# Kernel optimization log

Measured on AMD Instinct MI355X. Metric: run time of the kernel, lower is better.

## Reference

```python
import jax, jax.numpy as jnp
import numpy as np
from jax import lax

EPS = 1e-5

def setup_inputs() -> dict:
    key = jax.random.key(0)
    k1, k2, k3, k4, k5, k6 = jax.random.split(key, 6)
    x = jax.random.normal(k1, (1, 64, 31, 96, 96), dtype=jnp.float32)
    # small init scale keeps gate pre-activations in a sane range
    w = jax.random.normal(k2, (256, 64, 3, 3, 3), dtype=jnp.float32) * 0.05
    gamma = jax.random.uniform(k3, (256,), dtype=jnp.float32)
    beta = jax.random.normal(k4, (256,), dtype=jnp.float32) * 0.1
    mean = jax.random.normal(k5, (256,), dtype=jnp.float32) * 0.1
    var = jax.random.uniform(k6, (256,), dtype=jnp.float32) + 0.5
    return {"x": x, "w": w, "gamma": gamma, "beta": beta, "mean": mean, "var": var}

def _bcast(p):
    return p[None, :, None, None, None]

def reference(x, w, gamma, beta, mean, var):
    # Conv3d (bias=False), stride 1, padding 1, NCDHW
    gates = lax.conv_general_dilated(
        x, w, window_strides=(1, 1, 1), padding=[(1, 1)] * 3,
        dimension_numbers=("NCDHW", "OIDHW", "NCDHW"))
    # BatchNorm3d (inference, running stats)
    scale = gamma * lax.rsqrt(var + EPS)
    gates = gates * _bcast(scale) + _bcast(beta - mean * scale)
    C = 64  # out_channels
    Wx = jnp.tanh(gates[:, 0 * C:1 * C])
    ft = jax.nn.sigmoid(gates[:, 1 * C:2 * C])
    rt = jax.nn.sigmoid(gates[:, 2 * C:3 * C])
    X = jnp.tanh(gates[:, 3 * C:4 * C])  # act == 'tanh'
    # time axis (dim 2) to front: (D, B, C, H, W)
    Wt = jnp.moveaxis(Wx, 2, 0)
    Ft = jnp.moveaxis(ft, 2, 0)
    Rt = jnp.moveaxis(rt, 2, 0)
    Xt = jnp.moveaxis(X, 2, 0)
    # t = 0: Ct = 1 - ft (note: Wx unused at first step, per source)
    C0 = 1.0 - Ft[0]
    h0 = Rt[0] * C0 + (1.0 - Rt[0]) * Xt[0]
    def step(Ct, inp):
        wx, f, r, xx = inp
        Ct = f * Ct + (1.0 - f) * wx
        ht = r * Ct + (1.0 - r) * xx
        return Ct, ht
    _, hs = lax.scan(step, C0, (Wt[1:], Ft[1:], Rt[1:], Xt[1:]))
    hts = jnp.concatenate([h0[None], hs], axis=0)  # (D,B,C,H,W)
    return jnp.moveaxis(hts, 0, 2)  # (B,C,D,H,W)
```

## Files before the change

kernel.cpp:

```cpp
#include <hip/hip_runtime.h>
#include <cstddef>

#define CI_  64
#define CO_  256
#define DD_  31
#define HH_  96
#define WW_  96
#define HW_  (HH_*WW_)
#define DHW_ (DD_*HW_)
#define EPSV 1e-5f

#define PD_   33
#define PH_   98
#define PW_   98
#define PHW_  9604
#define PDHW_ 316932

#define S_COL 8
#define S_CIG 144
#define S_ROW 1152
#define S_DD  11520
#define NTASK 4320
#define NTASKP 4352
#define XH_N  (NTASKP*8)

#define NTILE 72
#define NBLK  (NTILE*DD_)
#define GSP   128

typedef _Float16 half8   __attribute__((ext_vector_type(8)));
typedef _Float16 half4v  __attribute__((ext_vector_type(4)));
typedef float    float4v __attribute__((ext_vector_type(4)));

__device__ __forceinline__ void gl_lds16(const _Float16* g, _Float16* l) {
  __builtin_amdgcn_global_load_lds(
      (const __attribute__((address_space(1))) unsigned int*)(g),
      (__attribute__((address_space(3))) unsigned int*)(l), 16, 0, 0);
}

__global__ __launch_bounds__(256) void repack_w_k(const float* __restrict__ w,
                                                  _Float16* __restrict__ wr2) {
  int idx = blockIdx.x * 256 + threadIdx.x;
  if (idx >= 55296) return;
  int lw   = idx & 15;
  int quad = (idx >> 4) & 3;
  int cog  = (idx >> 6) & 15;
  int tkc  = idx >> 10;
  int kc   = tkc & 1;
  int t    = tkc >> 1;
  int co   = cog * 16 + lw;
  int cib  = kc * 32 + quad * 8;
  half8 v;
#pragma unroll
  for (int s = 0; s < 8; s++)
    v[s] = (_Float16)w[(size_t)co * 1728 + (size_t)(cib + s) * 27 + t];
  *(half8*)(wr2 + (size_t)idx * 8) = v;
}

__global__ __launch_bounds__(256) void pad_zero_k(_Float16* __restrict__ xt) {
  int p = blockIdx.x * 256 + threadIdx.x;
  if (p >= PDHW_) return;
  int pd  = p / PHW_;
  int rem = p - pd * PHW_;
  int ph  = rem / PW_;
  int pw  = rem - ph * PW_;
  bool in = (pd >= 1) & (pd <= DD_) & (ph >= 1) & (ph <= HH_) & (pw >= 1) & (pw <= WW_);
  if (in) return;
  half8 z = (half8)(_Float16)0.f;
#pragma unroll
  for (int cig = 0; cig < 8; cig++)
    *(half8*)(xt + ((size_t)cig * PDHW_ + p) * 8) = z;
}

__global__ __launch_bounds__(256) void transpose_x_k(const float* __restrict__ x,
                                                     _Float16* __restrict__ xt) {
  int idx = blockIdx.x * 256 + threadIdx.x;
  if (idx >= 31 * 96 * 24) return;
  int wq  = idx % 24;
  int rem = idx / 24;
  int h   = rem % 96;
  int d   = rem / 96;
  const float* xp = x + (size_t)d * HW_ + (size_t)h * WW_ + wq * 4;
  size_t p0 = (size_t)(d + 1) * PHW_ + (size_t)(h + 1) * PW_ + (wq * 4 + 1);
#pragma unroll 1
  for (int cig = 0; cig < 8; cig++) {
    float4 vv[8];
#pragma unroll
    for (int s = 0; s < 8; s++)
      vv[s] = *(const float4*)(xp + (size_t)(cig * 8 + s) * DHW_);
#pragma unroll
    for (int k = 0; k < 4; k++) {
      half8 o;
#pragma unroll
      for (int s = 0; s < 8; s++) o[s] = (_Float16)(&vv[s].x)[k];
      *(half8*)(xt + ((size_t)cig * PDHW_ + p0 + k) * 8) = o;
    }
  }
}

__global__ __launch_bounds__(512, 4) void conv_mfma_k(
    const _Float16* __restrict__ xt, const _Float16* __restrict__ wr2,
    const float* __restrict__ gamma, const float* __restrict__ beta,
    const float* __restrict__ mean, const float* __restrict__ var,
    _Float16* __restrict__ gates)
{
  __shared__ _Float16 xh[XH_N];

  const int bid  = blockIdx.x;
  const int flat = (bid & 7) * 279 + (bid >> 3);
  const int d    = flat / NTILE;
  const int bx   = flat - d * NTILE;
  const int wti  = bx % 6;
  const int hti  = bx / 6;
  const int h0   = hti * 8, w0 = wti * 16;

  const int tid  = threadIdx.x;
  const int lane = tid & 63;
  const int wave = __builtin_amdgcn_readfirstlane(tid >> 6);
  const int wm   = wave >> 2;
  const int wn   = wave & 3;
  const int lw   = lane & 15;
  const int quad = lane >> 4;

#pragma unroll 1
  for (int it = 0; it < 9; ++it) {
    const int wb = it * 512 + wave * 64;
    if (wb < NTASKP) {
      const int task = wb + lane;
      const int tt   = task < NTASK ? task : (NTASK - 1);
      int col = tt % 18;
      int rc  = tt / 18;
      int cig = rc & 7;
      int dr  = rc >> 3;
      int dd  = dr / 10;
      int row = dr - dd * 10;
      const _Float16* g = xt + (((size_t)cig * PDHW_ + (size_t)(d + dd) * PHW_ +
                                 (size_t)(h0 + row) * PW_ + (w0 + col)) << 3);
      gl_lds16(g, xh + (size_t)wb * 8);
    }
  }

  float4v acc[4][4];
#pragma unroll
  for (int m = 0; m < 4; m++)
#pragma unroll
    for (int j = 0; j < 4; j++) acc[m][j] = (float4v)0.f;

  __syncthreads();

  const int abase0 = quad * S_CIG + lw * S_COL + (wm * 4) * S_ROW;

#define LOADB(bf, s)                                                          \
  {                                                                           \
    const int t9_ = (s) / 6, sub_ = (s) - 6 * t9_;                            \
    const int kc_ = sub_ / 3, kw_ = sub_ - 3 * kc_;                           \
    const int t_  = t9_ * 3 + kw_;                                            \
    const _Float16* bp_ =                                                     \
        wr2 + (((size_t)((t_ * 2 + kc_) * 16 + wn * 4)) << 9) + (lane << 3);  \
    bf[0] = *(const half8*)(bp_);                                             \
    bf[1] = *(const half8*)(bp_ + (1 << 9));                                  \
    bf[2] = *(const half8*)(bp_ + (2 << 9));                                  \
    bf[3] = *(const half8*)(bp_ + (3 << 9));                                  \
  }

#define STEP(s, bf)                                                           \
  {                                                                           \
    const int t9_ = (s) / 6, sub_ = (s) - 6 * t9_;                            \
    const int kc_ = sub_ / 3, kw_ = sub_ - 3 * kc_;                           \
    const int kd_ = t9_ / 3, kh_ = t9_ - 3 * kd_;                             \
    const int ab_ = abase0 + kd_ * S_DD + kh_ * S_ROW + kc_ * (4 * S_CIG) +   \
                    kw_ * S_COL;                                              \
    half8 af0 = *(const half8*)(xh + ab_);                                    \
    half8 af1 = *(const half8*)(xh + ab_ + S_ROW);                            \
    half8 af2 = *(const half8*)(xh + ab_ + 2 * S_ROW);                        \
    half8 af3 = *(const half8*)(xh + ab_ + 3 * S_ROW);                        \
    __builtin_amdgcn_s_setprio(1);                                            \
    _Pragma("unroll")                                                         \
    for (int j = 0; j < 4; ++j) {                                             \
      acc[0][j] = __builtin_amdgcn_mfma_f32_16x16x32_f16(af0, bf[j], acc[0][j], 0, 0, 0); \
      acc[1][j] = __builtin_amdgcn_mfma_f32_16x16x32_f16(af1, bf[j], acc[1][j], 0, 0, 0); \
      acc[2][j] = __builtin_amdgcn_mfma_f32_16x16x32_f16(af2, bf[j], acc[2][j], 0, 0, 0); \
      acc[3][j] = __builtin_amdgcn_mfma_f32_16x16x32_f16(af3, bf[j], acc[3][j], 0, 0, 0); \
    }                                                                         \
    __builtin_amdgcn_s_setprio(0);                                            \
  }

  half8 bfa[4], bfb[4];
  LOADB(bfa, 0)
#pragma unroll 1
  for (int i = 0; i < 27; ++i) {
    const int s0 = 2 * i;
    LOADB(bfb, s0 + 1)
    STEP(s0, bfa)
    if (i < 26) LOADB(bfa, s0 + 2)
    STEP(s0 + 1, bfb)
  }
#undef LOADB
#undef STEP

  _Float16* gb = gates + ((size_t)(d * NTILE + bx) * 256) * GSP;
#pragma unroll
  for (int j = 0; j < 4; j++) {
    const int co = wn * 64 + j * 16 + lw;
    const float s  = gamma[co] * rsqrtf(var[co] + EPSV);
    const float bb = fmaf(-mean[co], s, beta[co]);
#pragma unroll
    for (int m = 0; m < 4; m++) {
      half4v hv;
#pragma unroll
      for (int reg = 0; reg < 4; reg++)
        hv[reg] = (_Float16)fmaf(acc[m][j][reg], s, bb);
      *(half4v*)(gb + (size_t)co * GSP + (wm * 4 + m) * 16 + quad * 4) = hv;
    }
  }
}

__device__ __forceinline__ float tanh_f(float v) {
  float t = __expf(-2.f * fabsf(v));
  return copysignf((1.f - t) * __builtin_amdgcn_rcpf(1.f + t), v);
}
__device__ __forceinline__ float sigm_f(float v) {
  return __builtin_amdgcn_rcpf(1.f + __expf(-v));
}

__global__ __launch_bounds__(256) void recurrence_k(const _Float16* __restrict__ gates,
                                                    float* __restrict__ out) {
  const int idx = blockIdx.x * 256 + threadIdx.x;
  const int q   = idx & 31;
  const int t2  = idx >> 5;
  const int c   = t2 / NTILE;
  const int bx  = t2 - c * NTILE;
  const int hti = bx / 6, wti = bx - hti * 6;
  const int sp  = q * 4;
  const int h   = hti * 8 + (sp >> 4);
  const int w   = wti * 16 + (sp & 15);

  const size_t DSTR = (size_t)NTILE * 256 * GSP;
  const _Float16* g0 = gates + (size_t)bx * 256 * GSP + sp;
  float* op = out + (size_t)c * DHW_ + (size_t)h * WW_ + w;

#define LD(dv, gate) (*(const half4v*)(g0 + (size_t)(dv) * DSTR + (size_t)(c + ((gate) << 6)) * GSP))

  half4v cf = LD(0, 1), cr = LD(0, 2), cx = LD(0, 3);
  half4v nwx = LD(1, 0), nf = LD(1, 1), nr = LD(1, 2), nx = LD(1, 3);
  float C[4];
  {
    float4 st;
#pragma unroll
    for (int k = 0; k < 4; k++) {
      C[k] = 1.f - sigm_f((float)cf[k]);
      float r0 = sigm_f((float)cr[k]), x0 = tanh_f((float)cx[k]);
      (&st.x)[k] = fmaf(r0, C[k] - x0, x0);
    }
    *(float4*)op = st;
  }
#pragma unroll 1
  for (int d = 1; d < DD_; d++) {
    half4v cwx = nwx; cf = nf; cr = nr; cx = nx;
    if (d < DD_ - 1) {
      nwx = LD(d + 1, 0); nf = LD(d + 1, 1);
      nr  = LD(d + 1, 2); nx = LD(d + 1, 3);
    }
    float4 st;
#pragma unroll
    for (int k = 0; k < 4; k++) {
      float wx0 = tanh_f((float)cwx[k]);
      float f0  = sigm_f((float)cf[k]);
      float r0  = sigm_f((float)cr[k]);
      float x0  = tanh_f((float)cx[k]);
      C[k] = fmaf(f0, C[k] - wx0, wx0);
      (&st.x)[k] = fmaf(r0, C[k] - x0, x0);
    }
    *(float4*)(op + (size_t)d * HW_) = st;
  }
#undef LD
}

extern "C" void kernel_launch(void* const* d_in, const int* in_sizes, int n_in,
                              void* d_out, int out_size, void* d_ws, size_t ws_size,
                              hipStream_t stream) {
  const float* x     = (const float*)d_in[0];
  const float* w     = (const float*)d_in[1];
  const float* gamma = (const float*)d_in[2];
  const float* beta  = (const float*)d_in[3];
  const float* mean  = (const float*)d_in[4];
  const float* var   = (const float*)d_in[5];
  float* out = (float*)d_out;

  _Float16* wr2   = (_Float16*)d_ws;
  _Float16* xt    = (_Float16*)((char*)d_ws + 884736);
  _Float16* gates = (_Float16*)((char*)d_ws + 884736 + 40567296);

  repack_w_k<<<216, 256, 0, stream>>>(w, wr2);
  pad_zero_k<<<(PDHW_ + 255) / 256, 256, 0, stream>>>(xt);
  transpose_x_k<<<(31 * 96 * 24 + 255) / 256, 256, 0, stream>>>(x, xt);
  conv_mfma_k<<<NBLK, 512, 0, stream>>>(xt, wr2, gamma, beta, mean, var, gates);
  recurrence_k<<<(64 * NTILE * 32) / 256, 256, 0, stream>>>(gates, out);
}
```

Measured before the change: 421.5 us.

## Fuse prep kernels and move gate activations into conv epilogue with LDS-staged stores

Merges the weight repack, pad zeroing and input transpose into one launch that dispatches by block index. It moves the tanh/sigmoid activations from the recurrence kernel into the conv epilogue, where they run once per gate element rather than inside the serial time loop. Gate stores are staged through swizzled LDS so each lane writes contiguous half8 chunks to global memory, replacing scattered half4 writes. The epilogue gains an extra __syncthreads and LDS traffic, and activations are now rounded to fp16 after being computed rather than before.

```diff
diff --git a/kernel.cpp b/kernel.cpp
--- a/kernel.cpp
+++ b/kernel.cpp
@@ -28,6 +28,11 @@
 #define NBLK  (NTILE*DD_)
 #define GSP   128
 
+#define PREP_RB 216
+#define PREP_PB 1239
+#define PREP_TB 279
+#define PREP_NB (PREP_RB + PREP_PB + PREP_TB)
+
 typedef _Float16 half8   __attribute__((ext_vector_type(8)));
 typedef _Float16 half4v  __attribute__((ext_vector_type(4)));
 typedef float    float4v __attribute__((ext_vector_type(4)));
@@ -38,64 +43,71 @@
       (__attribute__((address_space(3))) unsigned int*)(l), 16, 0, 0);
 }
 
-__global__ __launch_bounds__(256) void repack_w_k(const float* __restrict__ w,
-                                                  _Float16* __restrict__ wr2) {
-  int idx = blockIdx.x * 256 + threadIdx.x;
-  if (idx >= 55296) return;
-  int lw   = idx & 15;
-  int quad = (idx >> 4) & 3;
-  int cog  = (idx >> 6) & 15;
-  int tkc  = idx >> 10;
-  int kc   = tkc & 1;
-  int t    = tkc >> 1;
-  int co   = cog * 16 + lw;
-  int cib  = kc * 32 + quad * 8;
-  half8 v;
-#pragma unroll
-  for (int s = 0; s < 8; s++)
-    v[s] = (_Float16)w[(size_t)co * 1728 + (size_t)(cib + s) * 27 + t];
-  *(half8*)(wr2 + (size_t)idx * 8) = v;
-}
-
-__global__ __launch_bounds__(256) void pad_zero_k(_Float16* __restrict__ xt) {
-  int p = blockIdx.x * 256 + threadIdx.x;
-  if (p >= PDHW_) return;
-  int pd  = p / PHW_;
-  int rem = p - pd * PHW_;
-  int ph  = rem / PW_;
-  int pw  = rem - ph * PW_;
-  bool in = (pd >= 1) & (pd <= DD_) & (ph >= 1) & (ph <= HH_) & (pw >= 1) & (pw <= WW_);
-  if (in) return;
-  half8 z = (half8)(_Float16)0.f;
-#pragma unroll
-  for (int cig = 0; cig < 8; cig++)
-    *(half8*)(xt + ((size_t)cig * PDHW_ + p) * 8) = z;
-}
-
-__global__ __launch_bounds__(256) void transpose_x_k(const float* __restrict__ x,
-                                                     _Float16* __restrict__ xt) {
-  int idx = blockIdx.x * 256 + threadIdx.x;
-  if (idx >= 31 * 96 * 24) return;
-  int wq  = idx % 24;
-  int rem = idx / 24;
-  int h   = rem % 96;
-  int d   = rem / 96;
-  const float* xp = x + (size_t)d * HW_ + (size_t)h * WW_ + wq * 4;
-  size_t p0 = (size_t)(d + 1) * PHW_ + (size_t)(h + 1) * PW_ + (wq * 4 + 1);
+__global__ __launch_bounds__(256) void prep_k(const float* __restrict__ w,
+                                              const float* __restrict__ x,
+                                              _Float16* __restrict__ wr2,
+                                              _Float16* __restrict__ xt) {
+  const int bid = blockIdx.x;
+  if (bid < PREP_RB) {
+    int idx = bid * 256 + threadIdx.x;
+    int lw   = idx & 15;
+    int quad = (idx >> 4) & 3;
+    int cog  = (idx >> 6) & 15;
+    int tkc  = idx >> 10;
+    int kc   = tkc & 1;
+    int t    = tkc >> 1;
+    int co   = cog * 16 + lw;
+    int cib  = kc * 32 + quad * 8;
+    half8 v;
+#pragma unroll
+    for (int s = 0; s < 8; s++)
+      v[s] = (_Float16)w[(size_t)co * 1728 + (size_t)(cib + s) * 27 + t];
+    *(half8*)(wr2 + (size_t)idx * 8) = v;
+  } else if (bid < PREP_RB + PREP_PB) {
+    int p = (bid - PREP_RB) * 256 + threadIdx.x;
+    if (p >= PDHW_) return;
+    int pd  = p / PHW_;
+    int rem = p - pd * PHW_;
+    int ph  = rem / PW_;
+    int pw  = rem - ph * PW_;
+    bool in = (pd >= 1) & (pd <= DD_) & (ph >= 1) & (ph <= HH_) & (pw >= 1) & (pw <= WW_);
+    if (in) return;
+    half8 z = (half8)(_Float16)0.f;
+#pragma unroll
+    for (int cig = 0; cig < 8; cig++)
+      *(half8*)(xt + ((size_t)cig * PDHW_ + p) * 8) = z;
+  } else {
+    int idx = (bid - PREP_RB - PREP_PB) * 256 + threadIdx.x;
+    if (idx >= 31 * 96 * 24) return;
+    int wq  = idx % 24;
+    int rem = idx / 24;
+    int h   = rem % 96;
+    int d   = rem / 96;
+    const float* xp = x + (size_t)d * HW_ + (size_t)h * WW_ + wq * 4;
+    size_t p0 = (size_t)(d + 1) * PHW_ + (size_t)(h + 1) * PW_ + (wq * 4 + 1);
 #pragma unroll 1
-  for (int cig = 0; cig < 8; cig++) {
-    float4 vv[8];
-#pragma unroll
-    for (int s = 0; s < 8; s++)
-      vv[s] = *(const float4*)(xp + (size_t)(cig * 8 + s) * DHW_);
-#pragma unroll
-    for (int k = 0; k < 4; k++) {
-      half8 o;
-#pragma unroll
-      for (int s = 0; s < 8; s++) o[s] = (_Float16)(&vv[s].x)[k];
-      *(half8*)(xt + ((size_t)cig * PDHW_ + p0 + k) * 8) = o;
-    }
-  }
+    for (int cig = 0; cig < 8; cig++) {
+      float4 vv[8];
+#pragma unroll
+      for (int s = 0; s < 8; s++)
+        vv[s] = *(const float4*)(xp + (size_t)(cig * 8 + s) * DHW_);
+#pragma unroll
+      for (int k = 0; k < 4; k++) {
+        half8 o;
+#pragma unroll
+        for (int s = 0; s < 8; s++) o[s] = (_Float16)(&vv[s].x)[k];
+        *(half8*)(xt + ((size_t)cig * PDHW_ + p0 + k) * 8) = o;
+      }
+    }
+  }
+}
+
+__device__ __forceinline__ float tanh_f(float v) {
+  float t = __expf(-2.f * fabsf(v));
+  return copysignf((1.f - t) * __builtin_amdgcn_rcpf(1.f + t), v);
+}
+__device__ __forceinline__ float sigm_f(float v) {
+  return __builtin_amdgcn_rcpf(1.f + __expf(-v));
 }
 
 __global__ __launch_bounds__(512, 4) void conv_mfma_k(
@@ -198,29 +210,38 @@
 #undef LOADB
 #undef STEP
 
-  _Float16* gb = gates + ((size_t)(d * NTILE + bx) * 256) * GSP;
+  __syncthreads();
+
+  _Float16* wt = xh + wave * 4096;
+  const bool istanh = (wn == 0) || (wn == 3);
 #pragma unroll
   for (int j = 0; j < 4; j++) {
-    const int co = wn * 64 + j * 16 + lw;
+    const int co  = wn * 64 + j * 16 + lw;
+    const int col = j * 16 + lw;
     const float s  = gamma[co] * rsqrtf(var[co] + EPSV);
     const float bb = fmaf(-mean[co], s, beta[co]);
+    const int key = (col & 7) << 3;
 #pragma unroll
     for (int m = 0; m < 4; m++) {
       half4v hv;
 #pragma unroll
-      for (int reg = 0; reg < 4; reg++)
-        hv[reg] = (_Float16)fmaf(acc[m][j][reg], s, bb);
-      *(half4v*)(gb + (size_t)co * GSP + (wm * 4 + m) * 16 + quad * 4) = hv;
-    }
-  }
-}
-
-__device__ __forceinline__ float tanh_f(float v) {
-  float t = __expf(-2.f * fabsf(v));
-  return copysignf((1.f - t) * __builtin_amdgcn_rcpf(1.f + t), v);
-}
-__device__ __forceinline__ float sigm_f(float v) {
-  return __builtin_amdgcn_rcpf(1.f + __expf(-v));
+      for (int reg = 0; reg < 4; reg++) {
+        float v = fmaf(acc[m][j][reg], s, bb);
+        float a;
+        if (istanh) a = tanh_f(v); else a = sigm_f(v);
+        hv[reg] = (_Float16)a;
+      }
+      *(half4v*)(wt + col * 64 + ((m * 16 + quad * 4) ^ key)) = hv;
+    }
+  }
+  _Float16* gb = gates + ((size_t)(d * NTILE + bx) * 256 + wn * 64) * GSP + wm * 64;
+  const int rb = (lane & 7) * 8;
+#pragma unroll
+  for (int s8 = 0; s8 < 8; s8++) {
+    const int col = s8 * 8 + (lane >> 3);
+    half8 rv = *(const half8*)(wt + col * 64 + (rb ^ ((col & 7) << 3)));
+    *(half8*)(gb + (size_t)col * GSP + rb) = rv;
+  }
 }
 
 __global__ __launch_bounds__(256) void recurrence_k(const _Float16* __restrict__ gates,
@@ -248,8 +269,8 @@
     float4 st;
 #pragma unroll
     for (int k = 0; k < 4; k++) {
-      C[k] = 1.f - sigm_f((float)cf[k]);
-      float r0 = sigm_f((float)cr[k]), x0 = tanh_f((float)cx[k]);
+      C[k] = 1.f - (float)cf[k];
+      float r0 = (float)cr[k], x0 = (float)cx[k];
       (&st.x)[k] = fmaf(r0, C[k] - x0, x0);
     }
     *(float4*)op = st;
@@ -264,10 +285,7 @@
     float4 st;
 #pragma unroll
     for (int k = 0; k < 4; k++) {
-      float wx0 = tanh_f((float)cwx[k]);
-      float f0  = sigm_f((float)cf[k]);
-      float r0  = sigm_f((float)cr[k]);
-      float x0  = tanh_f((float)cx[k]);
+      float wx0 = (float)cwx[k], f0 = (float)cf[k], r0 = (float)cr[k], x0 = (float)cx[k];
       C[k] = fmaf(f0, C[k] - wx0, wx0);
       (&st.x)[k] = fmaf(r0, C[k] - x0, x0);
     }
@@ -291,9 +309,7 @@
   _Float16* xt    = (_Float16*)((char*)d_ws + 884736);
   _Float16* gates = (_Float16*)((char*)d_ws + 884736 + 40567296);
 
-  repack_w_k<<<216, 256, 0, stream>>>(w, wr2);
-  pad_zero_k<<<(PDHW_ + 255) / 256, 256, 0, stream>>>(xt);
-  transpose_x_k<<<(31 * 96 * 24 + 255) / 256, 256, 0, stream>>>(x, xt);
+  prep_k<<<PREP_NB, 256, 0, stream>>>(w, x, wr2, xt);
   conv_mfma_k<<<NBLK, 512, 0, stream>>>(xt, wr2, gamma, beta, mean, var, gates);
   recurrence_k<<<(64 * NTILE * 32) / 256, 256, 0, stream>>>(gates, out);
 }
```

Result: no change. 422.8 us (+0.3%).
